# Kernel tuning notes

Hardware: AMD Instinct MI355X
Metric: run time of the kernel (lower is better)

The kernel has to match this reference:

```python
import jax, jax.numpy as jnp
import numpy as np

GROUP_SIZES = [16, 16, 16, 16]
K = 2
TEMPERATURE = 1.0
NEG = float(np.finfo(np.float32).min)  # torch.finfo(dtype).min


def setup_inputs() -> dict:
    key = jax.random.key(0)
    k1, k2, k3 = jax.random.split(key, 3)
    B, S, D, E, G = 8, 4096, 1024, 64, len(GROUP_SIZES)
    x = jax.random.normal(k1, (B, S, D), dtype=jnp.float32)
    W_group = jax.random.normal(k2, (G, D), dtype=jnp.float32) * 0.02
    W_expert = jax.random.normal(k3, (E, D), dtype=jnp.float32) * 0.02
    return {"x": x, "W_group": W_group, "W_expert": W_expert}


def reference(x, W_group, W_expert):
    E = W_expert.shape[0]
    # group id of each expert (contiguous ranges) -- static
    expert_group = jnp.asarray(np.repeat(np.arange(len(GROUP_SIZES)), GROUP_SIZES))  # [E]

    # gate logits (no bias), temperature scaling
    expert_logits = jnp.einsum('bsd,ed->bse', x, W_expert) * (1.0 / TEMPERATURE)  # [B,S,E]
    group_logits = jnp.einsum('bsd,gd->bsg', x, W_group)                          # [B,S,G]
    group_probs = jax.nn.softmax(group_logits, axis=-1)
    g_idx = jnp.argmax(group_probs, axis=-1)                                      # [B,S]

    # mask experts outside the selected group's contiguous range
    mask = expert_group[None, None, :] != g_idx[..., None]                        # [B,S,E] bool
    mdt = mask.astype(expert_logits.dtype)
    masked_logits = mdt * NEG + (1.0 - mdt) * expert_logits

    probs_full = jax.nn.softmax(masked_logits, axis=-1)                           # [B,S,E]
    topk_vals, idx = jax.lax.top_k(masked_logits, K)                              # [B,S,K]
    scores = jax.nn.softmax(topk_vals, axis=-1)

    # aux stats (no_grad in original)
    importance = jax.lax.stop_gradient(jnp.mean(probs_full, axis=(0, 1)))         # [E]
    counts = jnp.zeros((E,), probs_full.dtype).at[idx.reshape(-1)].add(1.0)       # [E]
    load = counts / jnp.maximum(jnp.sum(counts), 1.0)
    return (idx, scores, probs_full, importance, load)
```

## Files before the change

kernel.cpp:

```cpp
#include <hip/hip_runtime.h>
#include <math.h>

#define TOKENS   32768
#define DDIM     1024
#define TPB      32
#define NBLOCKS  (TOKENS / TPB)

#define OFF_SCORES 65536
#define OFF_PROBS  131072
#define OFF_IMP    2228224
#define OFF_LOAD   2228288

#define NSLOT 32

typedef __attribute__((ext_vector_type(8))) short  short8;
typedef __attribute__((ext_vector_type(4))) float  f32x4;
typedef __attribute__((ext_vector_type(4))) int    intx4;

__device__ __attribute__((aligned(16))) short wfrag[32 * 5 * 3 * 64 * 8];

__device__ inline unsigned rne_hi(float x) {
  unsigned u = __float_as_uint(x);
  unsigned r = u + 0x7fffu + ((u >> 16) & 1u);
  return r & 0xffff0000u;
}

__device__ inline void split3(const float* xv, short8& f1, short8& f2, short8& f3) {
  int o1[4], o2[4], o3[4];
  #pragma unroll
  for (int p = 0; p < 4; ++p) {
    float x0 = xv[2*p], x1 = xv[2*p+1];
    unsigned h0 = rne_hi(x0), h1 = rne_hi(x1);
    o1[p] = (int)((h0 >> 16) | (h1 & 0xffff0000u));
    float r0 = x0 - __uint_as_float(h0);
    float r1 = x1 - __uint_as_float(h1);
    unsigned g0 = rne_hi(r0), g1 = rne_hi(r1);
    o2[p] = (int)((g0 >> 16) | (g1 & 0xffff0000u));
    float s0 = r0 - __uint_as_float(g0);
    float s1 = r1 - __uint_as_float(g1);
    unsigned w0 = rne_hi(s0), w1 = rne_hi(s1);
    o3[p] = (int)((w0 >> 16) | (w1 & 0xffff0000u));
  }
  intx4 t1 = {o1[0], o1[1], o1[2], o1[3]};
  intx4 t2 = {o2[0], o2[1], o2[2], o2[3]};
  intx4 t3 = {o3[0], o3[1], o3[2], o3[3]};
  f1 = __builtin_bit_cast(short8, t1);
  f2 = __builtin_bit_cast(short8, t2);
  f3 = __builtin_bit_cast(short8, t3);
}

__global__ void prep_kernel(const float* __restrict__ Wg, const float* __restrict__ We) {
  const int nt   = blockIdx.x >> 5;
  const int ks   = blockIdx.x & 31;
  const int lane = threadIdx.x & 63;
  const int row  = nt * 16 + (lane & 15);
  const int k0   = ks * 32 + (lane >> 4) * 8;
  float xv[8];
  #pragma unroll
  for (int j = 0; j < 8; ++j) {
    float v = 0.f;
    if (row < 64)      v = We[(size_t)row * DDIM + k0 + j];
    else if (row < 68) v = Wg[(size_t)(row - 64) * DDIM + k0 + j];
    xv[j] = v;
  }
  short8 f1, f2, f3;
  split3(xv, f1, f2, f3);
  short8* dst = (short8*)wfrag + (((size_t)ks * 5 + nt) * 3) * 64 + lane;
  dst[0]   = f1;
  dst[64]  = f2;
  dst[128] = f3;
}

__global__ __launch_bounds__(128)
__attribute__((amdgpu_waves_per_eu(2)))
void router_kernel(const float* __restrict__ x,
                   float* __restrict__ out,
                   float* __restrict__ ws) {
  __shared__ __attribute__((aligned(16))) float el[TPB * 88];
  __shared__ int cnt[64];
  const int tid    = threadIdx.x;
  const int lane   = tid & 63;
  const int khalf  = tid >> 6;
  const int quad   = lane >> 4;
  const int m      = lane & 15;
  const int tokblk = blockIdx.x * TPB;

  if (tid < 64) cnt[tid] = 0;

  const float* apb = x + (size_t)(tokblk + m) * DDIM + khalf * 512 + quad * 8;

  f32x4 ahi[2][5], alo[2][5];
  #pragma unroll
  for (int mt = 0; mt < 2; ++mt)
    #pragma unroll
    for (int nt = 0; nt < 5; ++nt) { ahi[mt][nt] = 0.f; alo[mt][nt] = 0.f; }

  float4 cur[4], nxt[4];
  #pragma unroll
  for (int mt = 0; mt < 2; ++mt) {
    const float* p = apb + (size_t)(mt * 16) * DDIM;
    cur[mt * 2]     = *(const float4*)(p);
    cur[mt * 2 + 1] = *(const float4*)(p + 4);
  }

  for (int ks = 0; ks < 16; ++ks) {
    const short8* bp = (const short8*)wfrag + ((size_t)(khalf * 16 + ks) * 15) * 64 + lane;
    short8 fb[5][3];
    #pragma unroll
    for (int nt = 0; nt < 5; ++nt) {
      fb[nt][0] = bp[nt * 192];
      fb[nt][1] = bp[nt * 192 + 64];
      fb[nt][2] = bp[nt * 192 + 128];
    }
    const int kpf = (ks + 1 < 16) ? (ks + 1) : 15;
    #pragma unroll
    for (int mt = 0; mt < 2; ++mt) {
      const float* p = apb + (size_t)(mt * 16) * DDIM + kpf * 32;
      nxt[mt * 2]     = *(const float4*)(p);
      nxt[mt * 2 + 1] = *(const float4*)(p + 4);
    }
    short8 fa[2][3];
    #pragma unroll
    for (int mt = 0; mt < 2; ++mt) {
      float av[8] = {cur[mt*2].x, cur[mt*2].y, cur[mt*2].z, cur[mt*2].w,
                     cur[mt*2+1].x, cur[mt*2+1].y, cur[mt*2+1].z, cur[mt*2+1].w};
      split3(av, fa[mt][0], fa[mt][1], fa[mt][2]);
    }
    #pragma unroll
    for (int nt = 0; nt < 5; ++nt)
      #pragma unroll
      for (int mt = 0; mt < 2; ++mt) {
        ahi[mt][nt] = __builtin_amdgcn_mfma_f32_16x16x32_bf16(fa[mt][0], fb[nt][0], ahi[mt][nt], 0, 0, 0);
        f32x4 c = alo[mt][nt];
        c = __builtin_amdgcn_mfma_f32_16x16x32_bf16(fa[mt][0], fb[nt][1], c, 0, 0, 0);
        c = __builtin_amdgcn_mfma_f32_16x16x32_bf16(fa[mt][1], fb[nt][0], c, 0, 0, 0);
        c = __builtin_amdgcn_mfma_f32_16x16x32_bf16(fa[mt][1], fb[nt][1], c, 0, 0, 0);
        c = __builtin_amdgcn_mfma_f32_16x16x32_bf16(fa[mt][0], fb[nt][2], c, 0, 0, 0);
        c = __builtin_amdgcn_mfma_f32_16x16x32_bf16(fa[mt][2], fb[nt][0], c, 0, 0, 0);
        c = __builtin_amdgcn_mfma_f32_16x16x32_bf16(fa[mt][1], fb[nt][2], c, 0, 0, 0);
        c = __builtin_amdgcn_mfma_f32_16x16x32_bf16(fa[mt][2], fb[nt][1], c, 0, 0, 0);
        alo[mt][nt] = c;
      }
    #pragma unroll
    for (int i = 0; i < 4; ++i) cur[i] = nxt[i];
  }

  if (khalf == 1) {
    #pragma unroll
    for (int mt = 0; mt < 2; ++mt)
      #pragma unroll
      for (int nt = 0; nt < 5; ++nt)
        #pragma unroll
        for (int r = 0; r < 4; ++r)
          el[(mt * 16 + quad * 4 + r) * 88 + nt * 16 + m] = ahi[mt][nt][r] + alo[mt][nt][r];
  }
  __syncthreads();
  if (khalf == 0) {
    #pragma unroll
    for (int mt = 0; mt < 2; ++mt)
      #pragma unroll
      for (int nt = 0; nt < 5; ++nt)
        #pragma unroll
        for (int r = 0; r < 4; ++r) {
          const int idx = (mt * 16 + quad * 4 + r) * 88 + nt * 16 + m;
          el[idx] += ahi[mt][nt][r] + alo[mt][nt][r];
        }
  }
  __syncthreads();

  if (tid < TPB) {
    const int t = tid;
    float* row = el + t * 88;
    const float g0 = row[64], g1 = row[65], g2 = row[66], g3 = row[67];
    int g = 0; float gb = g0;
    if (g1 > gb) { g = 1; gb = g1; }
    if (g2 > gb) { g = 2; gb = g2; }
    if (g3 > gb) { g = 3; gb = g3; }
    const int base = g << 4;
    float l[16];
    #pragma unroll
    for (int e = 0; e < 16; ++e) l[e] = row[base + e];
    int i1 = 0; float v1 = l[0];
    #pragma unroll
    for (int e = 1; e < 16; ++e) if (l[e] > v1) { i1 = e; v1 = l[e]; }
    int i2 = -1; float v2 = 0.f;
    #pragma unroll
    for (int e = 0; e < 16; ++e) {
      if (e == i1) continue;
      if (i2 < 0 || l[e] > v2) { i2 = e; v2 = l[e]; }
    }
    float pr[16]; float s = 0.f;
    #pragma unroll
    for (int e = 0; e < 16; ++e) { pr[e] = expf(l[e] - v1); s += pr[e]; }
    const float inv = 1.f / s;
    #pragma unroll
    for (int c = 0; c < 64; ++c) row[c] = 0.f;
    #pragma unroll
    for (int e = 0; e < 16; ++e) row[base + e] = pr[e] * inv;
    const size_t T = (size_t)tokblk + t;
    out[2*T]     = (float)(base + i1);
    out[2*T + 1] = (float)(base + i2);
    const float e2 = expf(v2 - v1);
    const float si = 1.f / (1.f + e2);
    out[OFF_SCORES + 2*T]     = si;
    out[OFF_SCORES + 2*T + 1] = e2 * si;
    atomicAdd(&cnt[base + i1], 1);
    atomicAdd(&cnt[base + i2], 1);
  }
  __syncthreads();

  for (int i = tid; i < TPB * 64; i += 128) {
    const int t = i >> 6, c = i & 63;
    out[OFF_PROBS + (((size_t)(tokblk + t)) << 6) + c] = el[t * 88 + c];
  }
  if (tid < 64) {
    const int e = tid;
    float s = 0.f;
    #pragma unroll 4
    for (int t = 0; t < TPB; ++t) s += el[t * 88 + e];
    const int slot = (blockIdx.x & (NSLOT - 1)) * 128;
    atomicAdd(&ws[slot + e], s);
    atomicAdd(&ws[slot + 64 + e], (float)cnt[e]);
  }
}

__global__ void finalize_kernel(const float* __restrict__ ws, float* __restrict__ out) {
  const int e = threadIdx.x;
  if (e < 64) {
    float imp = 0.f, cf = 0.f;
    #pragma unroll
    for (int s = 0; s < NSLOT; ++s) {
      imp += ws[s * 128 + e];
      cf  += ws[s * 128 + 64 + e];
    }
    out[OFF_IMP  + e] = imp * (1.0f / 32768.0f);
    out[OFF_LOAD + e] = cf  * (1.0f / 65536.0f);
  }
}

extern "C" void kernel_launch(void* const* d_in, const int* in_sizes, int n_in,
                              void* d_out, int out_size, void* d_ws, size_t ws_size,
                              hipStream_t stream) {
  (void)in_sizes; (void)n_in; (void)out_size; (void)ws_size;
  const float* x  = (const float*)d_in[0];
  const float* Wg = (const float*)d_in[1];
  const float* We = (const float*)d_in[2];
  float* out = (float*)d_out;
  float* ws  = (float*)d_ws;
  hipMemsetAsync(d_ws, 0, NSLOT * 128 * sizeof(float), stream);
  hipLaunchKernelGGL(prep_kernel, dim3(160), dim3(64), 0, stream, Wg, We);
  hipLaunchKernelGGL(router_kernel, dim3(NBLOCKS), dim3(128), 0, stream, x, out, ws);
  hipLaunchKernelGGL(finalize_kernel, dim3(1), dim3(64), 0, stream, ws, out);
}
```

Before: 220.6 us.

## Double block token tile and stage shared weight fragments in LDS

After: 208.4 us. -5.5%, faster.

```diff
diff --git a/kernel.cpp b/kernel.cpp
--- a/kernel.cpp
+++ b/kernel.cpp
@@ -3,7 +3,7 @@
 
 #define TOKENS   32768
 #define DDIM     1024
-#define TPB      32
+#define TPB      64
 #define NBLOCKS  (TOKENS / TPB)
 
 #define OFF_SCORES 65536
@@ -11,7 +11,7 @@
 #define OFF_IMP    2228224
 #define OFF_LOAD   2228288
 
-#define NSLOT 32
+#define NSLOT 16
 
 typedef __attribute__((ext_vector_type(8))) short  short8;
 typedef __attribute__((ext_vector_type(4))) float  f32x4;
@@ -71,23 +71,27 @@
   dst[128] = f3;
 }
 
-__global__ __launch_bounds__(128)
+__global__ __launch_bounds__(256)
 __attribute__((amdgpu_waves_per_eu(2)))
 void router_kernel(const float* __restrict__ x,
                    float* __restrict__ out,
                    float* __restrict__ ws) {
   __shared__ __attribute__((aligned(16))) float el[TPB * 88];
+  __shared__ __attribute__((aligned(16))) short8 bstage[30 * 64];
   __shared__ int cnt[64];
   const int tid    = threadIdx.x;
   const int lane   = tid & 63;
-  const int khalf  = tid >> 6;
+  const int wv     = tid >> 6;
+  const int khalf  = wv >> 1;
+  const int mhalf  = wv & 1;
   const int quad   = lane >> 4;
   const int m      = lane & 15;
   const int tokblk = blockIdx.x * TPB;
 
   if (tid < 64) cnt[tid] = 0;
 
-  const float* apb = x + (size_t)(tokblk + m) * DDIM + khalf * 512 + quad * 8;
+  const float* apb = x + (size_t)(tokblk + mhalf * 32 + m) * DDIM + khalf * 512 + quad * 8;
+  const short8* wsrc = (const short8*)wfrag;
 
   f32x4 ahi[2][5], alo[2][5];
   #pragma unroll
@@ -103,14 +107,42 @@
     cur[mt * 2 + 1] = *(const float4*)(p + 4);
   }
 
+  short8 breg[8];
+  #pragma unroll
+  for (int j = 0; j < 8; ++j) {
+    const int c = wv + 4 * j;
+    if (c < 30) {
+      const int ksg = (c < 15) ? 0 : 16;
+      const int fr  = (c < 15) ? c : c - 15;
+      breg[j] = wsrc[((size_t)ksg * 15 + fr) * 64 + lane];
+    }
+  }
+  #pragma unroll
+  for (int j = 0; j < 8; ++j) {
+    const int c = wv + 4 * j;
+    if (c < 30) bstage[c * 64 + lane] = breg[j];
+  }
+  __syncthreads();
+
   for (int ks = 0; ks < 16; ++ks) {
-    const short8* bp = (const short8*)wfrag + ((size_t)(khalf * 16 + ks) * 15) * 64 + lane;
     short8 fb[5][3];
     #pragma unroll
     for (int nt = 0; nt < 5; ++nt) {
-      fb[nt][0] = bp[nt * 192];
-      fb[nt][1] = bp[nt * 192 + 64];
-      fb[nt][2] = bp[nt * 192 + 128];
+      const short8* bp = &bstage[(khalf * 15 + nt * 3) * 64 + lane];
+      fb[nt][0] = bp[0];
+      fb[nt][1] = bp[64];
+      fb[nt][2] = bp[128];
+    }
+    if (ks < 15) {
+      #pragma unroll
+      for (int j = 0; j < 8; ++j) {
+        const int c = wv + 4 * j;
+        if (c < 30) {
+          const int ksg = (c < 15) ? (ks + 1) : (16 + ks + 1);
+          const int fr  = (c < 15) ? c : c - 15;
+          breg[j] = wsrc[((size_t)ksg * 15 + fr) * 64 + lane];
+        }
+      }
     }
     const int kpf = (ks + 1 < 16) ? (ks + 1) : 15;
     #pragma unroll
@@ -119,30 +151,37 @@
       nxt[mt * 2]     = *(const float4*)(p);
       nxt[mt * 2 + 1] = *(const float4*)(p + 4);
     }
-    short8 fa[2][3];
     #pragma unroll
     for (int mt = 0; mt < 2; ++mt) {
       float av[8] = {cur[mt*2].x, cur[mt*2].y, cur[mt*2].z, cur[mt*2].w,
                      cur[mt*2+1].x, cur[mt*2+1].y, cur[mt*2+1].z, cur[mt*2+1].w};
-      split3(av, fa[mt][0], fa[mt][1], fa[mt][2]);
-    }
-    #pragma unroll
-    for (int nt = 0; nt < 5; ++nt)
-      #pragma unroll
-      for (int mt = 0; mt < 2; ++mt) {
-        ahi[mt][nt] = __builtin_amdgcn_mfma_f32_16x16x32_bf16(fa[mt][0], fb[nt][0], ahi[mt][nt], 0, 0, 0);
+      short8 fa0, fa1, fa2;
+      split3(av, fa0, fa1, fa2);
+      #pragma unroll
+      for (int nt = 0; nt < 5; ++nt) {
+        ahi[mt][nt] = __builtin_amdgcn_mfma_f32_16x16x32_bf16(fa0, fb[nt][0], ahi[mt][nt], 0, 0, 0);
         f32x4 c = alo[mt][nt];
-        c = __builtin_amdgcn_mfma_f32_16x16x32_bf16(fa[mt][0], fb[nt][1], c, 0, 0, 0);
-        c = __builtin_amdgcn_mfma_f32_16x16x32_bf16(fa[mt][1], fb[nt][0], c, 0, 0, 0);
-        c = __builtin_amdgcn_mfma_f32_16x16x32_bf16(fa[mt][1], fb[nt][1], c, 0, 0, 0);
-        c = __builtin_amdgcn_mfma_f32_16x16x32_bf16(fa[mt][0], fb[nt][2], c, 0, 0, 0);
-        c = __builtin_amdgcn_mfma_f32_16x16x32_bf16(fa[mt][2], fb[nt][0], c, 0, 0, 0);
-        c = __builtin_amdgcn_mfma_f32_16x16x32_bf16(fa[mt][1], fb[nt][2], c, 0, 0, 0);
-        c = __builtin_amdgcn_mfma_f32_16x16x32_bf16(fa[mt][2], fb[nt][1], c, 0, 0, 0);
+        c = __builtin_amdgcn_mfma_f32_16x16x32_bf16(fa0, fb[nt][1], c, 0, 0, 0);
+        c = __builtin_amdgcn_mfma_f32_16x16x32_bf16(fa1, fb[nt][0], c, 0, 0, 0);
+        c = __builtin_amdgcn_mfma_f32_16x16x32_bf16(fa1, fb[nt][1], c, 0, 0, 0);
+        c = __builtin_amdgcn_mfma_f32_16x16x32_bf16(fa0, fb[nt][2], c, 0, 0, 0);
+        c = __builtin_amdgcn_mfma_f32_16x16x32_bf16(fa2, fb[nt][0], c, 0, 0, 0);
+        c = __builtin_amdgcn_mfma_f32_16x16x32_bf16(fa1, fb[nt][2], c, 0, 0, 0);
+        c = __builtin_amdgcn_mfma_f32_16x16x32_bf16(fa2, fb[nt][1], c, 0, 0, 0);
         alo[mt][nt] = c;
       }
+    }
     #pragma unroll
     for (int i = 0; i < 4; ++i) cur[i] = nxt[i];
+    if (ks < 15) {
+      __syncthreads();
+      #pragma unroll
+      for (int j = 0; j < 8; ++j) {
+        const int c = wv + 4 * j;
+        if (c < 30) bstage[c * 64 + lane] = breg[j];
+      }
+      __syncthreads();
+    }
   }
 
   if (khalf == 1) {
@@ -152,7 +191,7 @@
       for (int nt = 0; nt < 5; ++nt)
         #pragma unroll
         for (int r = 0; r < 4; ++r)
-          el[(mt * 16 + quad * 4 + r) * 88 + nt * 16 + m] = ahi[mt][nt][r] + alo[mt][nt][r];
+          el[(mhalf * 32 + mt * 16 + quad * 4 + r) * 88 + nt * 16 + m] = ahi[mt][nt][r] + alo[mt][nt][r];
   }
   __syncthreads();
   if (khalf == 0) {
@@ -162,7 +201,7 @@
       for (int nt = 0; nt < 5; ++nt)
         #pragma unroll
         for (int r = 0; r < 4; ++r) {
-          const int idx = (mt * 16 + quad * 4 + r) * 88 + nt * 16 + m;
+          const int idx = (mhalf * 32 + mt * 16 + quad * 4 + r) * 88 + nt * 16 + m;
           el[idx] += ahi[mt][nt][r] + alo[mt][nt][r];
         }
   }
@@ -209,7 +248,7 @@
   }
   __syncthreads();
 
-  for (int i = tid; i < TPB * 64; i += 128) {
+  for (int i = tid; i < TPB * 64; i += 256) {
     const int t = i >> 6, c = i & 63;
     out[OFF_PROBS + (((size_t)(tokblk + t)) << 6) + c] = el[t * 88 + c];
   }
@@ -249,6 +288,6 @@
   float* ws  = (float*)d_ws;
   hipMemsetAsync(d_ws, 0, NSLOT * 128 * sizeof(float), stream);
   hipLaunchKernelGGL(prep_kernel, dim3(160), dim3(64), 0, stream, Wg, We);
-  hipLaunchKernelGGL(router_kernel, dim3(NBLOCKS), dim3(128), 0, stream, x, out, ws);
+  hipLaunchKernelGGL(router_kernel, dim3(NBLOCKS), dim3(256), 0, stream, x, out, ws);
   hipLaunchKernelGGL(finalize_kernel, dim3(1), dim3(64), 0, stream, ws, out);
 }
```
